# Kernel tuning notes

Hardware: AMD Instinct MI355X
Metric: run time of the kernel (lower is better)

The kernel has to match this reference:

```python
import jax, jax.numpy as jnp
import numpy as np

B, N, C, NH = 4, 2304, 256, 8
HD = C // NH            # head dim = 32
HS = WS = 48            # H = W = sqrt(N)
RADIUS = 3.0
MLP_HID = 4 * C
SCALE = HD ** (-0.5)
NEG = -1e9              # stands in for -inf (identical softmax up to fp eps)
EPS = 1e-6


def spatial_mask():
    # get_spatial_mask: cdist of (y, x) grid coords, -inf where dist > radius
    yy, xx = jnp.meshgrid(jnp.arange(HS), jnp.arange(WS), indexing='ij')
    coords = jnp.stack([yy, xx], -1).reshape(-1, 2).astype(jnp.float32)  # [N, 2]
    d2 = jnp.sum((coords[:, None, :] - coords[None, :, :]) ** 2, -1)     # [N, N]
    return jnp.where(d2 > RADIUS * RADIUS, NEG, 0.0)


def layernorm(x, g, b):
    mu = jnp.mean(x, -1, keepdims=True)
    var = jnp.mean((x - mu) ** 2, -1, keepdims=True)
    return (x - mu) * jax.lax.rsqrt(var + EPS) * g + b


def setup_inputs() -> dict:
    key = jax.random.key(0)
    ks = jax.random.split(key, 16)
    s = 0.02
    return {
        'x':    jax.random.normal(ks[0], (B, N, C), jnp.float32),
        'x_kv': jax.random.normal(ks[1], (B, N, C), jnp.float32),
        'Wq': jax.random.normal(ks[2], (C, C), jnp.float32) * s,
        'bq': jnp.zeros((C,), jnp.float32),
        'Wk': jax.random.normal(ks[3], (C, C), jnp.float32) * s,
        'bk': jnp.zeros((C,), jnp.float32),
        'Wv': jax.random.normal(ks[4], (C, C), jnp.float32) * s,
        'bv': jnp.zeros((C,), jnp.float32),
        'Wp': jax.random.normal(ks[5], (C, C), jnp.float32) * s,
        'bp': jnp.zeros((C,), jnp.float32),
        'g1': jnp.ones((C,), jnp.float32),
        'b1': jnp.zeros((C,), jnp.float32),
        'g2': jnp.ones((C,), jnp.float32),
        'b2': jnp.zeros((C,), jnp.float32),
        'W1': jax.random.normal(ks[6], (C, MLP_HID), jnp.float32) * s,
        'bm1': jnp.zeros((MLP_HID,), jnp.float32),
        'W2': jax.random.normal(ks[7], (MLP_HID, C), jnp.float32) * s,
        'bm2': jnp.zeros((C,), jnp.float32),
    }


def reference(x, x_kv, Wq, bq, Wk, bk, Wv, bv, Wp, bp,
              g1, b1, g2, b2, W1, bm1, W2, bm2):
    mask = spatial_mask()                                  # [N, N]
    h = layernorm(x, g1, b1)
    hkv = layernorm(x_kv, g1, b1)
    q = (h @ Wq + bq).reshape(B, N, NH, HD)
    k = (hkv @ Wk + bk).reshape(B, N, NH, HD)
    v = (hkv @ Wv + bv).reshape(B, N, NH, HD)
    scores = jnp.einsum('bqhd,bkhd->bhqk', q, k) * SCALE + mask
    attn = jax.nn.softmax(scores, axis=-1)
    out = jnp.einsum('bhqk,bkhd->bqhd', attn, v).reshape(B, N, C)
    x = x + out @ Wp + bp
    m = layernorm(x, g2, b2)
    x = x + jax.nn.gelu(m @ W1 + bm1, approximate=False) @ W2 + bm2
    return x
```

## Files before the change

kernel.cpp:

```cpp
#include <hip/hip_runtime.h>
#include <hip/hip_fp16.h>
#include <math.h>

#define BB 4
#define NN 2304
#define CC 256
#define HS 48
#define HID 1024
#define BNROWS (BB * NN)
#define ATTN_SCALE 0.17677669529663687f

typedef _Float16 f16;
typedef __attribute__((ext_vector_type(2))) _Float16 h2;
typedef __attribute__((ext_vector_type(8))) _Float16 h8;
typedef __attribute__((ext_vector_type(4))) float f4;

#define GLLS16(g, l)                                                        \
    __builtin_amdgcn_global_load_lds(                                       \
        (const __attribute__((address_space(1))) unsigned int*)(g),         \
        (__attribute__((address_space(3))) unsigned int*)(l), 16, 0, 0)
#define WAIT_VM0()   asm volatile("s_waitcnt vmcnt(0)" ::: "memory")
#define WAIT_VM5()   asm volatile("s_waitcnt vmcnt(5)" ::: "memory")
#define WAIT_VM6()   asm volatile("s_waitcnt vmcnt(6)" ::: "memory")
#define WAIT_LGKM0() asm volatile("s_waitcnt lgkmcnt(0)" ::: "memory")

static __device__ __forceinline__ float wave_sum64(float v) {
    v += __shfl_xor(v, 32, 64);
    v += __shfl_xor(v, 16, 64);
    v += __shfl_xor(v, 8, 64);
    v += __shfl_xor(v, 4, 64);
    v += __shfl_xor(v, 2, 64);
    v += __shfl_xor(v, 1, 64);
    return v;
}

static __device__ __forceinline__ int xcd_swizzle_lin() {
    const int gx = (int)gridDim.x;
    const int lin = (int)blockIdx.y * gx + (int)blockIdx.x;
    const int nwg = gx * (int)gridDim.y;
    return (nwg & 7) ? lin : ((lin & 7) * (nwg >> 3) + (lin >> 3));
}

__global__ __launch_bounds__(256) void prep_ln1_kernel(
    const float* __restrict__ x, const float* __restrict__ xkv,
    const float* __restrict__ Wq, const float* __restrict__ Wk,
    const float* __restrict__ Wv, const float* __restrict__ Wp,
    const float* __restrict__ W1, const float* __restrict__ W2,
    const float* __restrict__ bq, const float* __restrict__ bk,
    const float* __restrict__ bv,
    const float* __restrict__ g, const float* __restrict__ be,
    f16* __restrict__ WqkvT, f16* __restrict__ WpT,
    f16* __restrict__ W1T, f16* __restrict__ W2T, float* __restrict__ bqkv,
    f16* __restrict__ hq, f16* __restrict__ hkv)
{
    __shared__ float tt[32][33];
    int bx = blockIdx.x;
    const int tid = threadIdx.x;
    if (bx < 768) {
        const float* src; f16* dst; int K, N;
        if (bx < 64)        { src = Wq; dst = WqkvT;           K = 256;  N = 256; }
        else if (bx < 128)  { src = Wk; dst = WqkvT + 65536;   K = 256;  N = 256;  bx -= 64; }
        else if (bx < 192)  { src = Wv; dst = WqkvT + 131072;  K = 256;  N = 256;  bx -= 128; }
        else if (bx < 256)  { src = Wp; dst = WpT;             K = 256;  N = 256;  bx -= 192; }
        else if (bx < 512)  { src = W1; dst = W1T;             K = 256;  N = 1024; bx -= 256; }
        else                { src = W2; dst = W2T;             K = 1024; N = 256;  bx -= 512; }
        const int tN = N >> 5;
        const int kt = bx / tN, nt = bx - kt * tN;
        const int rr = tid >> 5, cc = tid & 31;
#pragma unroll
        for (int j = 0; j < 4; ++j)
            tt[rr + 8 * j][cc] = src[(size_t)(kt * 32 + rr + 8 * j) * N + nt * 32 + cc];
        __syncthreads();
#pragma unroll
        for (int j = 0; j < 4; ++j)
            dst[(size_t)(nt * 32 + rr + 8 * j) * K + kt * 32 + cc] = (f16)tt[cc][rr + 8 * j];
        return;
    }
    if (bx == 768) {
        if (tid < 256) {
            bqkv[tid]       = bq[tid];
            bqkv[tid + 256] = bk[tid];
            bqkv[tid + 512] = bv[tid];
        }
        return;
    }
    const int r = (bx - 769) * 4 + (tid >> 6);
    const int lane = tid & 63;
    const float* src; f16* dst;
    if (r < BNROWS) { src = x + (size_t)r * CC;              dst = hq + (size_t)r * CC; }
    else { src = xkv + (size_t)(r - BNROWS) * CC; dst = hkv + (size_t)(r - BNROWS) * CC; }
    const float4 v = ((const float4*)src)[lane];
    const float mu = wave_sum64(v.x + v.y + v.z + v.w) * (1.0f / CC);
    const float d0 = v.x - mu, d1 = v.y - mu, d2 = v.z - mu, d3 = v.w - mu;
    const float var = wave_sum64(d0 * d0 + d1 * d1 + d2 * d2 + d3 * d3) * (1.0f / CC);
    const float rs = rsqrtf(var + 1e-6f);
    const float4 g4 = ((const float4*)g)[lane];
    const float4 b4 = ((const float4*)be)[lane];
    h2 o01 = (h2){(f16)(d0 * rs * g4.x + b4.x), (f16)(d1 * rs * g4.y + b4.y)};
    h2 o23 = (h2){(f16)(d2 * rs * g4.z + b4.z), (f16)(d3 * rs * g4.w + b4.w)};
    ((h2*)dst)[lane * 2] = o01;
    ((h2*)dst)[lane * 2 + 1] = o23;
}

template <bool GELU, int RESID, bool OUTF32, bool QKV>
__global__ __launch_bounds__(256, 4) void gemm_wave(
    const f16* __restrict__ Aq, const f16* __restrict__ Akv,
    const f16* __restrict__ Bt, const float* __restrict__ bias,
    const void* __restrict__ resid, void* __restrict__ out1,
    void* __restrict__ outkv, int N, int K)
{
    __shared__ f16 lds[4 * 6144];
    const int tid = threadIdx.x;
    const int wid = tid >> 6, lane = tid & 63;
    const int ln15 = lane & 15, quad = lane >> 4;
    const int jr = lane >> 2, js = lane & 3;
    f16* slot = lds + wid * 6144;
    const int sl = xcd_swizzle_lin();
    const int gx = (int)gridDim.x;
    const int bx = sl % gx, by = sl / gx;
    const int n0 = bx * 64;
    const int m0 = (by * 4 + wid) * 32;
    const f16* Ap = QKV ? (n0 < 256 ? Aq : Akv) : Aq;

    size_t ga[2], gb[4];
#pragma unroll
    for (int i = 0; i < 2; ++i) {
        const int r = i * 16 + jr;
        const int q = (js - (r >> 1)) & 3;
        ga[i] = (size_t)(m0 + r) * K + q * 8;
    }
#pragma unroll
    for (int i = 0; i < 4; ++i) {
        const int r = i * 16 + jr;
        const int q = (js - (r >> 1)) & 3;
        gb[i] = (size_t)(n0 + r) * K + q * 8;
    }
    int aoff[2], boff[4];
#pragma unroll
    for (int mt = 0; mt < 2; ++mt) {
        const int r = mt * 16 + ln15;
        aoff[mt] = (r * 4 + ((quad + (r >> 1)) & 3)) * 16;
    }
#pragma unroll
    for (int nt = 0; nt < 4; ++nt) {
        const int r = nt * 16 + ln15;
        boff[nt] = (r * 4 + ((quad + (r >> 1)) & 3)) * 16;
    }

    f4 acc[2][4];
#pragma unroll
    for (int i = 0; i < 2; ++i)
#pragma unroll
        for (int j = 0; j < 4; ++j) acc[i][j] = (f4){0.f, 0.f, 0.f, 0.f};

    {
        f16* Al = slot;
        f16* Bl = slot + 1024;
#pragma unroll
        for (int i = 0; i < 2; ++i) GLLS16(Ap + ga[i], Al + i * 512);
#pragma unroll
        for (int i = 0; i < 4; ++i) GLLS16(Bt + gb[i], Bl + i * 512);
    }

    int cur = 0;
    for (int k0 = 0; k0 < K; k0 += 32) {
        const bool more = (k0 + 32 < K);
        f16* Ac = slot + cur * 3072;
        f16* Bc = Ac + 1024;
        if (more) {
            f16* An = slot + (cur ^ 1) * 3072;
            f16* Bn = An + 1024;
            WAIT_LGKM0();
#pragma unroll
            for (int i = 0; i < 2; ++i) GLLS16(Ap + ga[i] + k0 + 32, An + i * 512);
#pragma unroll
            for (int i = 0; i < 4; ++i) GLLS16(Bt + gb[i] + k0 + 32, Bn + i * 512);
            WAIT_VM6();
        } else {
            WAIT_VM0();
        }
        h8 aF[2], bF[4];
#pragma unroll
        for (int nt = 0; nt < 4; ++nt)
            bF[nt] = *(const h8*)((const char*)Bc + boff[nt]);
#pragma unroll
        for (int mt = 0; mt < 2; ++mt)
            aF[mt] = *(const h8*)((const char*)Ac + aoff[mt]);
#pragma unroll
        for (int mt = 0; mt < 2; ++mt)
#pragma unroll
            for (int nt = 0; nt < 4; ++nt)
                acc[mt][nt] = __builtin_amdgcn_mfma_f32_16x16x32_f16(
                    aF[mt], bF[nt], acc[mt][nt], 0, 0, 0);
        cur ^= 1;
    }

    f16* qdst = nullptr; int qstr = 0, qn0 = 0;
    if (QKV) {
        if (n0 < 256) { qdst = (f16*)out1;  qstr = 256; qn0 = n0; }
        else          { qdst = (f16*)outkv; qstr = 512; qn0 = n0 - 256; }
    }
#pragma unroll
    for (int nt = 0; nt < 4; ++nt) {
        const int gn = n0 + nt * 16 + ln15;
        const float bs = bias[gn];
#pragma unroll
        for (int mt = 0; mt < 2; ++mt) {
#pragma unroll
            for (int r = 0; r < 4; ++r) {
                const int gm = m0 + mt * 16 + quad * 4 + r;
                float v = acc[mt][nt][r] + bs;
                if (GELU) v = 0.5f * v * (1.0f + erff(v * 0.70710678118654752f));
                if (RESID == 1) v += ((const float*)resid)[(size_t)gm * N + gn];
                if (RESID == 2) v += (float)((const f16*)resid)[(size_t)gm * N + gn];
                if (QKV) {
                    qdst[(size_t)gm * qstr + qn0 + nt * 16 + ln15] = (f16)v;
                } else if (OUTF32) {
                    ((float*)out1)[(size_t)gm * N + gn] = v;
                } else {
                    ((f16*)out1)[(size_t)gm * N + gn] = (f16)v;
                }
            }
        }
    }
}

__global__ __launch_bounds__(256, 4) void gemm_op_ln2(
    const f16* __restrict__ Aa, const f16* __restrict__ Bt,
    const float* __restrict__ bias, const float* __restrict__ xres,
    const float* __restrict__ g, const float* __restrict__ be,
    f16* __restrict__ x1, f16* __restrict__ m2)
{
    __shared__ f16 lds[4 * 5120];
    __shared__ float sred[16][4][2];
    const int tid = threadIdx.x;
    const int wid = tid >> 6, lane = tid & 63;
    const int ln15 = lane & 15, quad = lane >> 4;
    const int jr = lane >> 2, js = lane & 3;
    f16* slot = lds + wid * 5120;
    const int m0 = blockIdx.x * 16;
    const int n0 = wid * 64;
    const int K = 256;

    size_t ga, gb[4];
    {
        const int q = (js - (jr >> 1)) & 3;
        ga = (size_t)(m0 + jr) * K + q * 8;
    }
#pragma unroll
    for (int i = 0; i < 4; ++i) {
        const int r = i * 16 + jr;
        const int q = (js - (r >> 1)) & 3;
        gb[i] = (size_t)(n0 + r) * K + q * 8;
    }
    const int aoff = (ln15 * 4 + ((quad + (ln15 >> 1)) & 3)) * 16;
    int boff[4];
#pragma unroll
    for (int nt = 0; nt < 4; ++nt) {
        const int r = nt * 16 + ln15;
        boff[nt] = (r * 4 + ((quad + (r >> 1)) & 3)) * 16;
    }

    f4 acc[4];
#pragma unroll
    for (int j = 0; j < 4; ++j) acc[j] = (f4){0.f, 0.f, 0.f, 0.f};

    {
        f16* Al = slot;
        f16* Bl = slot + 512;
        GLLS16(Aa + ga, Al);
#pragma unroll
        for (int i = 0; i < 4; ++i) GLLS16(Bt + gb[i], Bl + i * 512);
    }
    int cur = 0;
    for (int k0 = 0; k0 < K; k0 += 32) {
        const bool more = (k0 + 32 < K);
        f16* Ac = slot + cur * 2560;
        f16* Bc = Ac + 512;
        if (more) {
            f16* An = slot + (cur ^ 1) * 2560;
            f16* Bn = An + 512;
            WAIT_LGKM0();
            GLLS16(Aa + ga + k0 + 32, An);
#pragma unroll
            for (int i = 0; i < 4; ++i) GLLS16(Bt + gb[i] + k0 + 32, Bn + i * 512);
            WAIT_VM5();
        } else {
            WAIT_VM0();
        }
        h8 aF, bF[4];
#pragma unroll
        for (int nt = 0; nt < 4; ++nt)
            bF[nt] = *(const h8*)((const char*)Bc + boff[nt]);
        aF = *(const h8*)((const char*)Ac + aoff);
#pragma unroll
        for (int nt = 0; nt < 4; ++nt)
            acc[nt] = __builtin_amdgcn_mfma_f32_16x16x32_f16(
                aF, bF[nt], acc[nt], 0, 0, 0);
        cur ^= 1;
    }

    float bsv[4], g2v[4], b2v[4];
#pragma unroll
    for (int nt = 0; nt < 4; ++nt) {
        const int gn = n0 + nt * 16 + ln15;
        bsv[nt] = bias[gn];
        g2v[nt] = g[gn];
        b2v[nt] = be[gn];
    }
    float s1[4], s2[4];
#pragma unroll
    for (int r = 0; r < 4; ++r) { s1[r] = 0.f; s2[r] = 0.f; }
#pragma unroll
    for (int r = 0; r < 4; ++r) {
        const int gm = m0 + quad * 4 + r;
#pragma unroll
        for (int nt = 0; nt < 4; ++nt) {
            const int gn = n0 + nt * 16 + ln15;
            float v = acc[nt][r] + bsv[nt] + xres[(size_t)gm * CC + gn];
            acc[nt][r] = v;
            x1[(size_t)gm * CC + gn] = (f16)v;
            s1[r] += v;
            s2[r] += v * v;
        }
    }
#pragma unroll
    for (int off = 1; off < 16; off <<= 1) {
#pragma unroll
        for (int r = 0; r < 4; ++r) {
            s1[r] += __shfl_xor(s1[r], off, 64);
            s2[r] += __shfl_xor(s2[r], off, 64);
        }
    }
    if (ln15 == 0) {
#pragma unroll
        for (int r = 0; r < 4; ++r) {
            const int rr = quad * 4 + r;
            sred[rr][wid][0] = s1[r];
            sred[rr][wid][1] = s2[r];
        }
    }
    __syncthreads();
#pragma unroll
    for (int r = 0; r < 4; ++r) {
        const int rr = quad * 4 + r;
        const int gm = m0 + rr;
        float a = 0.f, b = 0.f;
#pragma unroll
        for (int w = 0; w < 4; ++w) {
            a += sred[rr][w][0];
            b += sred[rr][w][1];
        }
        const float mu = a * (1.0f / CC);
        const float var = fmaxf(b * (1.0f / CC) - mu * mu, 0.0f);
        const float rs = rsqrtf(var + 1e-6f);
#pragma unroll
        for (int nt = 0; nt < 4; ++nt) {
            const int gn = n0 + nt * 16 + ln15;
            const float v = acc[nt][r];
            m2[(size_t)gm * CC + gn] = (f16)((v - mu) * rs * g2v[nt] + b2v[nt]);
        }
    }
}

template <int BN, int WGM, int WGN, bool GELU, bool FINAL>
__global__ __launch_bounds__(256, 2) void gemm_block(
    const f16* __restrict__ A, const f16* __restrict__ Bt,
    const float* __restrict__ bias, const f16* __restrict__ resid16,
    void* __restrict__ outv, int N, int K)
{
    constexpr int T = 8 + BN / 16;
    constexpr int BUFE = 128 * 32 + BN * 32;
    constexpr int MT = 128 / WGM / 16;
    constexpr int WM = 128 / WGM, WN = BN / WGN;
    __shared__ f16 lds[2 * BUFE];
    const int tid = threadIdx.x;
    const int wid = tid >> 6, lane = tid & 63;
    const int ln15 = lane & 15, quad = lane >> 4;
    const int jr = lane >> 2, js = lane & 3;
    const int wr = (WGN == 1) ? wid : (wid >> 1);
    const int wc = (WGN == 1) ? 0 : (wid & 1);

    const int sl = xcd_swizzle_lin();
    const int gx = (int)gridDim.x;
    const int m0 = (sl % gx) * 128;
    const int n0 = (sl / gx) * BN;

    const size_t gabase = (size_t)jr * K + (size_t)(((js - (jr >> 1)) & 3) * 8);

    int aoff[MT], boff[4];
#pragma unroll
    for (int mt = 0; mt < MT; ++mt) {
        const int rr = wr * WM + mt * 16 + ln15;
        aoff[mt] = (rr * 4 + ((quad + (rr >> 1)) & 3)) * 16;
    }
#pragma unroll
    for (int nt = 0; nt < 4; ++nt) {
        const int rr = wc * WN + nt * 16 + ln15;
        boff[nt] = 8192 + (rr * 4 + ((quad + (rr >> 1)) & 3)) * 16;
    }

    f4 acc[MT][4];
#pragma unroll
    for (int i = 0; i < MT; ++i)
#pragma unroll
        for (int j = 0; j < 4; ++j) acc[i][j] = (f4){0.f, 0.f, 0.f, 0.f};

#define GB_STAGE(dst, kk)                                                     \
    _Pragma("unroll")                                                         \
    for (int i = 0; i < T / 4; ++i) {                                         \
        const int g = wid + i * 4;                                            \
        const size_t rowoff =                                                 \
            (size_t)((g & 8) ? (n0 + (g & 7) * 16) : (m0 + g * 16)) * K;      \
        const f16* sp = ((g & 8) ? Bt : A) + rowoff + gabase + (kk);          \
        GLLS16(sp, (dst) + g * 512);                                          \
    }

    GB_STAGE(lds, 0);
    __syncthreads();
    int cur = 0;
    for (int k0 = 0; k0 < K; k0 += 32) {
        f16* bufc = lds + cur * BUFE;
        if (k0 + 32 < K) { GB_STAGE(lds + (cur ^ 1) * BUFE, k0 + 32); }
        h8 aF[MT], bF[4];
#pragma unroll
        for (int nt = 0; nt < 4; ++nt)
            bF[nt] = *(const h8*)((const char*)bufc + boff[nt]);
#pragma unroll
        for (int mt = 0; mt < MT; ++mt)
            aF[mt] = *(const h8*)((const char*)bufc + aoff[mt]);
#pragma unroll
        for (int mt = 0; mt < MT; ++mt)
#pragma unroll
            for (int nt = 0; nt < 4; ++nt)
                acc[mt][nt] = __builtin_amdgcn_mfma_f32_16x16x32_f16(
                    aF[mt], bF[nt], acc[mt][nt], 0, 0, 0);
        __syncthreads();
        cur ^= 1;
    }
#undef GB_STAGE

#pragma unroll
    for (int nt = 0; nt < 4; ++nt) {
        const int gn = n0 + wc * WN + nt * 16 + ln15;
        const float bs = bias[gn];
#pragma unroll
        for (int mt = 0; mt < MT; ++mt) {
#pragma unroll
            for (int r = 0; r < 4; ++r) {
                const int gm = m0 + wr * WM + mt * 16 + quad * 4 + r;
                float v = acc[mt][nt][r] + bs;
                if (GELU) v = 0.5f * v * (1.0f + erff(v * 0.70710678118654752f));
                if (FINAL) {
                    v += (float)resid16[(size_t)gm * N + gn];
                    ((float*)outv)[(size_t)gm * N + gn] = v;
                } else {
                    ((f16*)outv)[(size_t)gm * N + gn] = (f16)v;
                }
            }
        }
    }
}

__device__ __constant__ int ATT_DY[29] = {
    -3, -2, -2, -2, -2, -2, -1, -1, -1, -1, -1, 0, 0, 0, 0,
    0, 0, 0, 1, 1, 1, 1, 1, 2, 2, 2, 2, 2, 3};
__device__ __constant__ int ATT_DX[29] = {
    0, -2, -1, 0, 1, 2, -2, -1, 0, 1, 2, -3, -2, -1, 0,
    1, 2, 3, -2, -1, 0, 1, 2, -2, -1, 0, 1, 2, 0};

__global__ __launch_bounds__(128) void attn_tile_kernel(
    const f16* __restrict__ qf, const f16* __restrict__ kvf,
    f16* __restrict__ ao)
{
    __shared__ f16 ks[196][66];
    __shared__ f16 vs[196][66];
    const int tile = blockIdx.x, hp = blockIdx.y, b = blockIdx.z;
    const int ty0 = (tile / 6) * 8, tx0 = (tile - (tile / 6) * 6) * 8;
    const int tid = threadIdx.x;

    const int q = tid & 63, hh = tid >> 6;
    const int qy = q >> 3, qx = q & 7;
    const size_t qrow = (size_t)b * NN + (ty0 + qy) * HS + tx0 + qx;
    const f16* qp = qf + qrow * CC + hp * 64 + hh * 32;
    uint4 qa[4];
#pragma unroll
    for (int i = 0; i < 4; ++i) qa[i] = ((const uint4*)qp)[i];

#pragma unroll
    for (int bt = 0; bt < 5; ++bt) {
        uint4 v[5];
        int rr[5], sg[5];
#pragma unroll
        for (int j = 0; j < 5; ++j) {
            const int it = bt * 5 + j;
            const int idx = tid + it * 128;
            const int r = idx >> 4, seg = idx & 15;
            rr[j] = r; sg[j] = seg;
            const int ry = r / 14;
            const int gy = ty0 - 3 + ry, gx = tx0 - 3 + (r - ry * 14);
            uint4 val = {0u, 0u, 0u, 0u};
            const bool act = (it < 24) || (tid < 64);
            if (act && (unsigned)gy < HS && (unsigned)gx < HS) {
                const size_t rowb = ((size_t)b * NN + gy * HS + gx) * 512;
                const int ch = (seg < 8) ? (hp * 64 + seg * 8)
                                         : (256 + hp * 64 + (seg - 8) * 8);
                val = *(const uint4*)&kvf[rowb + ch];
            }
            v[j] = val;
        }
#pragma unroll
        for (int j = 0; j < 5; ++j) {
            const int it = bt * 5 + j;
            if (it == 24 && tid >= 64) continue;
            f16* dstp = (sg[j] < 8) ? &ks[rr[j]][(sg[j] & 7) * 8]
                                    : &vs[rr[j]][(sg[j] & 7) * 8];
            ((unsigned int*)dstp)[0] = v[j].x;
            ((unsigned int*)dstp)[1] = v[j].y;
            ((unsigned int*)dstp)[2] = v[j].z;
            ((unsigned int*)dstp)[3] = v[j].w;
        }
    }
    __syncthreads();

    const h2* q2 = (const h2*)qa;

    float s[29];
#pragma unroll
    for (int n = 0; n < 29; ++n) {
        const int dy = ATT_DY[n], dx = ATT_DX[n];
        const int r = (qy + 3 + dy) * 14 + qx + 3 + dx;
        const bool valid = (unsigned)(ty0 + qy + dy) < HS &&
                           (unsigned)(tx0 + qx + dx) < HS;
        float a = 0.0f;
        const h2* kp = (const h2*)&ks[r][hh * 32];
#pragma unroll
        for (int i = 0; i < 16; ++i)
            a = __builtin_amdgcn_fdot2(q2[i], kp[i], a, false);
        s[n] = valid ? a * ATTN_SCALE : -1e30f;
    }
    float m = s[0];
#pragma unroll
    for (int n = 1; n < 29; ++n) m = fmaxf(m, s[n]);
    float l = 0.0f;
#pragma unroll
    for (int n = 0; n < 29; ++n) { s[n] = __expf(s[n] - m); l += s[n]; }
    h2 a2[16];
#pragma unroll
    for (int i = 0; i < 16; ++i) a2[i] = (h2){(f16)0.f, (f16)0.f};
#pragma unroll
    for (int n = 0; n < 29; ++n) {
        const int dy = ATT_DY[n], dx = ATT_DX[n];
        const int r = (qy + 3 + dy) * 14 + qx + 3 + dx;
        const f16 pn = (f16)s[n];
        const h2 ph = (h2){pn, pn};
        const h2* vp = (const h2*)&vs[r][hh * 32];
#pragma unroll
        for (int i = 0; i < 16; ++i) a2[i] += ph * vp[i];
    }
    const float inv = 1.0f / l;
    uint4 ov[4];
    f16* oh = (f16*)ov;
#pragma unroll
    for (int i = 0; i < 16; ++i) {
        oh[2 * i]     = (f16)((float)a2[i][0] * inv);
        oh[2 * i + 1] = (f16)((float)a2[i][1] * inv);
    }
    uint4* dst = (uint4*)(ao + qrow * CC + hp * 64 + hh * 32);
#pragma unroll
    for (int i = 0; i < 4; ++i) dst[i] = ov[i];
}

extern "C" void kernel_launch(void* const* d_in, const int* in_sizes, int n_in,
                              void* d_out, int out_size, void* d_ws, size_t ws_size,
                              hipStream_t stream) {
    const float* x    = (const float*)d_in[0];
    const float* x_kv = (const float*)d_in[1];
    const float* Wq   = (const float*)d_in[2];
    const float* bq   = (const float*)d_in[3];
    const float* Wk   = (const float*)d_in[4];
    const float* bk   = (const float*)d_in[5];
    const float* Wv   = (const float*)d_in[6];
    const float* bv   = (const float*)d_in[7];
    const float* Wp   = (const float*)d_in[8];
    const float* bp   = (const float*)d_in[9];
    const float* g1   = (const float*)d_in[10];
    const float* b1   = (const float*)d_in[11];
    const float* g2   = (const float*)d_in[12];
    const float* b2   = (const float*)d_in[13];
    const float* W1   = (const float*)d_in[14];
    const float* bm1  = (const float*)d_in[15];
    const float* W2   = (const float*)d_in[16];
    const float* bm2  = (const float*)d_in[17];
    float* outp = (float*)d_out;

    f16* wsh = (f16*)d_ws;
    f16* WqkvT = wsh;
    f16* WpT   = wsh + 196608;
    f16* W1T   = wsh + 262144;
    f16* W2T   = wsh + 524288;
    float* bqkv = (float*)(wsh + 786432);
    f16* hq    = wsh + 787968;
    f16* hkv   = wsh + 3147264;
    f16* qf    = wsh + 5506560;
    f16* kvf   = wsh + 7865856;
    f16* ao    = hq;
    f16* x1    = hkv;
    f16* m2    = qf;
    f16* hidF  = kvf;
    const bool fused = ws_size >= (size_t)17303040 * sizeof(f16);

    prep_ln1_kernel<<<5377, 256, 0, stream>>>(
        x, x_kv, Wq, Wk, Wv, Wp, W1, W2, bq, bk, bv, g1, b1,
        WqkvT, WpT, W1T, W2T, bqkv, hq, hkv);
    gemm_wave<false, 0, false, true><<<dim3(12, 72), 256, 0, stream>>>(
        hq, hkv, WqkvT, bqkv, nullptr, qf, kvf, 768, 256);
    attn_tile_kernel<<<dim3(36, 4, BB), 128, 0, stream>>>(qf, kvf, ao);
    gemm_op_ln2<<<576, 256, 0, stream>>>(ao, WpT, bp, x, g2, b2, x1, m2);
    if (fused) {
        gemm_block<128, 2, 2, true, false><<<dim3(72, 8), 256, 0, stream>>>(
            m2, W1T, bm1, nullptr, hidF, HID, 256);
        gemm_block<64, 4, 1, false, true><<<dim3(72, 4), 256, 0, stream>>>(
            hidF, W2T, bm2, x1, outp, CC, 1024);
    } else {
        for (int b = 0; b < BB; ++b) {
            const size_t off = (size_t)b * NN * CC;
            gemm_block<128, 2, 2, true, false><<<dim3(18, 8), 256, 0, stream>>>(
                m2 + off, W1T, bm1, nullptr, hidF, HID, 256);
            gemm_block<64, 4, 1, false, true><<<dim3(18, 4), 256, 0, stream>>>(
                hidF, W2T, bm2, x1 + off, outp + off, CC, 1024);
        }
    }
    (void)in_sizes; (void)n_in; (void)out_size;
}
```

Baseline: 179.4 us.

## Generalize MLP GEMM tiling to BK=64 and shrink FC2 tile to 64x64

The MLP GEMM kernel now takes BM, BN and BK as template parameters. Each stage loads two 32-wide K chunks per barrier, which halves the number of syncthreads per K pass. The FC2 GEMM switches from 128x64 tiles to 64x64 tiles with twice as many blocks (one wave per 16 rows), aiming to fill more CUs. In exchange, LDS use per block grows and each wave gets less data reuse in FC2. Unused template options are also removed from gemm_wave.

```diff
diff --git a/kernel.cpp b/kernel.cpp
--- a/kernel.cpp
+++ b/kernel.cpp
@@ -102,12 +102,11 @@
     ((h2*)dst)[lane * 2 + 1] = o23;
 }
 
-template <bool GELU, int RESID, bool OUTF32, bool QKV>
+template <bool QKV>
 __global__ __launch_bounds__(256, 4) void gemm_wave(
     const f16* __restrict__ Aq, const f16* __restrict__ Akv,
     const f16* __restrict__ Bt, const float* __restrict__ bias,
-    const void* __restrict__ resid, void* __restrict__ out1,
-    void* __restrict__ outkv, int N, int K)
+    void* __restrict__ out1, void* __restrict__ outkv, int N, int K)
 {
     __shared__ f16 lds[4 * 6144];
     const int tid = threadIdx.x;
@@ -210,13 +209,8 @@
             for (int r = 0; r < 4; ++r) {
                 const int gm = m0 + mt * 16 + quad * 4 + r;
                 float v = acc[mt][nt][r] + bs;
-                if (GELU) v = 0.5f * v * (1.0f + erff(v * 0.70710678118654752f));
-                if (RESID == 1) v += ((const float*)resid)[(size_t)gm * N + gn];
-                if (RESID == 2) v += (float)((const f16*)resid)[(size_t)gm * N + gn];
                 if (QKV) {
                     qdst[(size_t)gm * qstr + qn0 + nt * 16 + ln15] = (f16)v;
-                } else if (OUTF32) {
-                    ((float*)out1)[(size_t)gm * N + gn] = v;
                 } else {
                     ((f16*)out1)[(size_t)gm * N + gn] = (f16)v;
                 }
@@ -363,41 +357,47 @@
     }
 }
 
-template <int BN, int WGM, int WGN, bool GELU, bool FINAL>
+template <int BM, int BN, int BK, int WGM, int WGN, bool GELU, bool FINAL>
 __global__ __launch_bounds__(256, 2) void gemm_block(
     const f16* __restrict__ A, const f16* __restrict__ Bt,
     const float* __restrict__ bias, const f16* __restrict__ resid16,
     void* __restrict__ outv, int N, int K)
 {
-    constexpr int T = 8 + BN / 16;
-    constexpr int BUFE = 128 * 32 + BN * 32;
-    constexpr int MT = 128 / WGM / 16;
-    constexpr int WM = 128 / WGM, WN = BN / WGN;
+    constexpr int A_G = BM / 16, B_G = BN / 16;
+    constexpr int NCH = BK / 32;
+    constexpr int T = (A_G + B_G) * NCH;
+    constexpr int BUFE = (BM + BN) * BK;
+    constexpr int WM = BM / WGM, WN = BN / WGN;
+    constexpr int MT = WM / 16;
+    static_assert(WN == 64, "epilogue assumes 4 n-frags of 16");
     __shared__ f16 lds[2 * BUFE];
     const int tid = threadIdx.x;
     const int wid = tid >> 6, lane = tid & 63;
     const int ln15 = lane & 15, quad = lane >> 4;
     const int jr = lane >> 2, js = lane & 3;
-    const int wr = (WGN == 1) ? wid : (wid >> 1);
-    const int wc = (WGN == 1) ? 0 : (wid & 1);
+    const int wr = wid / WGN, wc = wid % WGN;
 
     const int sl = xcd_swizzle_lin();
     const int gx = (int)gridDim.x;
-    const int m0 = (sl % gx) * 128;
+    const int m0 = (sl % gx) * BM;
     const int n0 = (sl / gx) * BN;
 
     const size_t gabase = (size_t)jr * K + (size_t)(((js - (jr >> 1)) & 3) * 8);
 
-    int aoff[MT], boff[4];
-#pragma unroll
-    for (int mt = 0; mt < MT; ++mt) {
-        const int rr = wr * WM + mt * 16 + ln15;
-        aoff[mt] = (rr * 4 + ((quad + (rr >> 1)) & 3)) * 16;
-    }
-#pragma unroll
-    for (int nt = 0; nt < 4; ++nt) {
-        const int rr = wc * WN + nt * 16 + ln15;
-        boff[nt] = 8192 + (rr * 4 + ((quad + (rr >> 1)) & 3)) * 16;
+    int aoff[NCH][MT], boff[NCH][4];
+#pragma unroll
+    for (int c = 0; c < NCH; ++c) {
+#pragma unroll
+        for (int mt = 0; mt < MT; ++mt) {
+            const int rr = wr * WM + mt * 16 + ln15;
+            aoff[c][mt] = c * (BM * 64) + (rr * 4 + ((quad + (rr >> 1)) & 3)) * 16;
+        }
+#pragma unroll
+        for (int nt = 0; nt < 4; ++nt) {
+            const int rr = wc * WN + nt * 16 + ln15;
+            boff[c][nt] = BM * BK * 2 + c * (BN * 64)
+                        + (rr * 4 + ((quad + (rr >> 1)) & 3)) * 16;
+        }
     }
 
     f4 acc[MT][4];
@@ -409,32 +409,46 @@
 #define GB_STAGE(dst, kk)                                                     \
     _Pragma("unroll")                                                         \
     for (int i = 0; i < T / 4; ++i) {                                         \
-        const int g = wid + i * 4;                                            \
-        const size_t rowoff =                                                 \
-            (size_t)((g & 8) ? (n0 + (g & 7) * 16) : (m0 + g * 16)) * K;      \
-        const f16* sp = ((g & 8) ? Bt : A) + rowoff + gabase + (kk);          \
-        GLLS16(sp, (dst) + g * 512);                                          \
+        const int gg = wid + i * 4;                                           \
+        const f16* base;                                                      \
+        int dofs, c;                                                          \
+        if (gg < A_G * NCH) {                                                 \
+            c = gg / A_G;                                                     \
+            const int g = gg - c * A_G;                                       \
+            base = A + (size_t)(m0 + g * 16) * K;                             \
+            dofs = c * (BM * 32) + g * 512;                                   \
+        } else {                                                              \
+            const int h = gg - A_G * NCH;                                     \
+            c = h / B_G;                                                      \
+            const int g = h - c * B_G;                                        \
+            base = Bt + (size_t)(n0 + g * 16) * K;                            \
+            dofs = BM * BK + c * (BN * 32) + g * 512;                         \
+        }                                                                     \
+        GLLS16(base + gabase + (kk) + c * 32, (dst) + dofs);                  \
     }
 
     GB_STAGE(lds, 0);
     __syncthreads();
     int cur = 0;
-    for (int k0 = 0; k0 < K; k0 += 32) {
+    for (int k0 = 0; k0 < K; k0 += BK) {
         f16* bufc = lds + cur * BUFE;
-        if (k0 + 32 < K) { GB_STAGE(lds + (cur ^ 1) * BUFE, k0 + 32); }
-        h8 aF[MT], bF[4];
-#pragma unroll
-        for (int nt = 0; nt < 4; ++nt)
-            bF[nt] = *(const h8*)((const char*)bufc + boff[nt]);
-#pragma unroll
-        for (int mt = 0; mt < MT; ++mt)
-            aF[mt] = *(const h8*)((const char*)bufc + aoff[mt]);
-#pragma unroll
-        for (int mt = 0; mt < MT; ++mt)
+        if (k0 + BK < K) { GB_STAGE(lds + (cur ^ 1) * BUFE, k0 + BK); }
+#pragma unroll
+        for (int c = 0; c < NCH; ++c) {
+            h8 aF[MT], bF[4];
 #pragma unroll
             for (int nt = 0; nt < 4; ++nt)
-                acc[mt][nt] = __builtin_amdgcn_mfma_f32_16x16x32_f16(
-                    aF[mt], bF[nt], acc[mt][nt], 0, 0, 0);
+                bF[nt] = *(const h8*)((const char*)bufc + boff[c][nt]);
+#pragma unroll
+            for (int mt = 0; mt < MT; ++mt)
+                aF[mt] = *(const h8*)((const char*)bufc + aoff[c][mt]);
+#pragma unroll
+            for (int mt = 0; mt < MT; ++mt)
+#pragma unroll
+                for (int nt = 0; nt < 4; ++nt)
+                    acc[mt][nt] = __builtin_amdgcn_mfma_f32_16x16x32_f16(
+                        aF[mt], bF[nt], acc[mt][nt], 0, 0, 0);
+        }
         __syncthreads();
         cur ^= 1;
     }
@@ -613,22 +627,26 @@
     prep_ln1_kernel<<<5377, 256, 0, stream>>>(
         x, x_kv, Wq, Wk, Wv, Wp, W1, W2, bq, bk, bv, g1, b1,
         WqkvT, WpT, W1T, W2T, bqkv, hq, hkv);
-    gemm_wave<false, 0, false, true><<<dim3(12, 72), 256, 0, stream>>>(
-        hq, hkv, WqkvT, bqkv, nullptr, qf, kvf, 768, 256);
+    gemm_wave<true><<<dim3(12, 72), 256, 0, stream>>>(
+        hq, hkv, WqkvT, bqkv, qf, kvf, 768, 256);
     attn_tile_kernel<<<dim3(36, 4, BB), 128, 0, stream>>>(qf, kvf, ao);
     gemm_op_ln2<<<576, 256, 0, stream>>>(ao, WpT, bp, x, g2, b2, x1, m2);
     if (fused) {
-        gemm_block<128, 2, 2, true, false><<<dim3(72, 8), 256, 0, stream>>>(
-            m2, W1T, bm1, nullptr, hidF, HID, 256);
-        gemm_block<64, 4, 1, false, true><<<dim3(72, 4), 256, 0, stream>>>(
-            hidF, W2T, bm2, x1, outp, CC, 1024);
+        gemm_block<128, 128, 64, 2, 2, true, false>
+            <<<dim3(72, 8), 256, 0, stream>>>(
+                m2, W1T, bm1, nullptr, hidF, HID, 256);
+        gemm_block<64, 64, 64, 4, 1, false, true>
+            <<<dim3(144, 4), 256, 0, stream>>>(
+                hidF, W2T, bm2, x1, outp, CC, 1024);
     } else {
         for (int b = 0; b < BB; ++b) {
             const size_t off = (size_t)b * NN * CC;
-            gemm_block<128, 2, 2, true, false><<<dim3(18, 8), 256, 0, stream>>>(
-                m2 + off, W1T, bm1, nullptr, hidF, HID, 256);
-            gemm_block<64, 4, 1, false, true><<<dim3(18, 4), 256, 0, stream>>>(
-                hidF, W2T, bm2, x1 + off, outp + off, CC, 1024);
+            gemm_block<128, 128, 64, 2, 2, true, false>
+                <<<dim3(18, 8), 256, 0, stream>>>(
+                    m2 + off, W1T, bm1, nullptr, hidF, HID, 256);
+            gemm_block<64, 64, 64, 4, 1, false, true>
+                <<<dim3(36, 4), 256, 0, stream>>>(
+                    hidF, W2T, bm2, x1 + off, outp + off, CC, 1024);
         }
     }
     (void)in_sizes; (void)n_in; (void)out_size;
```

Result: no change. 180.8 us (+0.8%).
